# Kernel tuning notes

Measured on AMD Instinct MI355X. Metric: run time of the kernel, lower is better.

## Reference

```python
import jax, jax.numpy as jnp
import numpy as np

ATT_SCALE = 1.0  # att_scale_factor


def setup_inputs() -> dict:
    key = jax.random.key(0)
    k1, k2, k3, k4, k5 = jax.random.split(key, 5)
    B, P, IMG_D, SEQ_D, H = 64, 576, 1024, 1024, 512
    seq_features = jax.random.normal(k1, (B, SEQ_D), dtype=jnp.float32)
    img_features = jax.random.normal(k2, (B, P, IMG_D), dtype=jnp.float32)
    # torch nn.Linear weights: [out_features, in_features], scaled to typical init magnitude
    W_seq = jax.random.normal(k3, (H, SEQ_D), dtype=jnp.float32) * (1.0 / np.sqrt(SEQ_D))
    W_img = jax.random.normal(k4, (H, IMG_D), dtype=jnp.float32) * (1.0 / np.sqrt(IMG_D))
    W_w = jax.random.normal(k5, (1, H), dtype=jnp.float32) * (1.0 / np.sqrt(H))
    return {"seq_features": seq_features, "img_features": img_features,
            "W_seq": W_seq, "W_img": W_img, "W_w": W_w}


def reference(seq_features, img_features, W_seq, W_img, W_w):
    # tanh(SeqTrans(seq)) broadcast over patch dim (avoids explicit .repeat)
    seq_h = jnp.tanh(jnp.einsum('bd,hd->bh', seq_features, W_seq))          # [B, H]
    img_h = jnp.tanh(jnp.einsum('bpd,hd->bph', img_features, W_img))        # [B, P, H]
    attend = seq_h[:, None, :] * img_h                                       # [B, P, H]
    # Dropout is Identity (att_dropout=None)
    scores = ATT_SCALE * jnp.einsum('bph,oh->bpo', attend, W_w)              # [B, P, 1]
    alpha = jax.nn.softmax(scores, axis=1)                                   # softmax over patches
    # weighted sum over patches; alpha broadcasts over channel dim (no .repeat needed)
    attended_img = jnp.sum(img_features * alpha, axis=1)                     # [B, IMG_D]
    return attended_img
```

## Files before the change

kernel.cpp:

```cpp
#include <hip/hip_runtime.h>
#include <hip/hip_bf16.h>

#define BB 64
#define PP 576
#define DD 1024
#define HH 512

typedef __attribute__((ext_vector_type(4))) float f32x4;
typedef __attribute__((ext_vector_type(8))) short bf16x8;

__device__ __forceinline__ unsigned short f2bf(float f) {
    union { float f; unsigned u; } v; v.f = f;
    unsigned r = v.u + 0x7FFF + ((v.u >> 16) & 1);
    return (unsigned short)(r >> 16);
}

__device__ __forceinline__ float fast_tanh(float x) {
    float e = __expf(2.f * x);
    return 1.f - 2.f / (e + 1.f);
}

__device__ __forceinline__ void gload16(const void* g, void* l) {
    __builtin_amdgcn_global_load_lds((const __attribute__((address_space(1))) unsigned int*)g,
                                     (__attribute__((address_space(3))) unsigned int*)l,
                                     16, 0, 0);
}

__global__ __launch_bounds__(256) void k_convert(const float* __restrict__ w,
                                                 unsigned short* __restrict__ o) {
    int i = (blockIdx.x * 256 + threadIdx.x) * 4;
    f32x4 v = *(const f32x4*)(w + i);
    ushort4 r;
    r.x = f2bf(v.x); r.y = f2bf(v.y); r.z = f2bf(v.z); r.w = f2bf(v.w);
    *(ushort4*)(o + i) = r;
}

__global__ __launch_bounds__(128) void k_seq(const float* __restrict__ seq,
                                             const float* __restrict__ W_seq,
                                             const float* __restrict__ W_w,
                                             float* __restrict__ g) {
    int b = blockIdx.x;
    int h = blockIdx.y * 128 + threadIdx.x;
    __shared__ float s_seq[DD];
    #pragma unroll
    for (int i = 0; i < 8; i++) s_seq[threadIdx.x + i * 128] = seq[b * DD + threadIdx.x + i * 128];
    __syncthreads();
    const float* wr = W_seq + (size_t)h * DD;
    float acc = 0.f;
    #pragma unroll 4
    for (int d = 0; d < DD; d += 4) {
        f32x4 w4 = *(const f32x4*)(wr + d);
        acc += w4.x * s_seq[d] + w4.y * s_seq[d + 1] + w4.z * s_seq[d + 2] + w4.w * s_seq[d + 3];
    }
    g[b * HH + h] = fast_tanh(acc) * W_w[h];
}

__global__ __launch_bounds__(256) void k_scores(const float* __restrict__ img,
                                                const unsigned short* __restrict__ Wb,
                                                const float* __restrict__ g,
                                                float* __restrict__ sp) {
    int b = blockIdx.y;
    int rt = blockIdx.x % 9;
    int ch = blockIdx.x / 9;
    int p0 = rt * 64;
    int h0 = ch * 256;
    int tid = threadIdx.x;
    int w = tid >> 6, lane = tid & 63;

    __shared__ unsigned short As[2][64 * 64];
    __shared__ unsigned short Bs[2][256 * 64];

    float gr[4];
    #pragma unroll
    for (int n = 0; n < 4; ++n) gr[n] = g[b * HH + h0 + w * 64 + n * 16 + (lane & 15)];

    f32x4 acc[4][4];
    #pragma unroll
    for (int m = 0; m < 4; m++)
        #pragma unroll
        for (int n = 0; n < 4; n++) acc[m][n] = (f32x4)0.f;

    int ar = tid >> 2;
    int ac = (tid & 3) * 16;
    const float* asrc = img + ((size_t)(b * PP + p0 + ar)) * DD + ac;
    int cp = (tid & 3) * 2;
    int aw0 = ar * 64 + ((cp ^ (ar & 7)) * 8);
    int aw1 = ar * 64 + (((cp + 1) ^ (ar & 7)) * 8);

    int brow_l = lane >> 3;
    int bchunk = lane & 7;

    auto stageB = [&](int bi, int kr) {
        int k0 = kr * 64;
        #pragma unroll
        for (int i = 0; i < 8; ++i) {
            int hr = (w * 8 + i) * 8 + brow_l;
            const unsigned short* src = Wb + (size_t)(h0 + hr) * DD + k0 + ((bchunk ^ (hr & 7)) * 8);
            gload16(src, &Bs[bi][(w * 8 + i) * 512]);
        }
    };
    auto packA = [&](int bi, f32x4 v0, f32x4 v1, f32x4 v2, f32x4 v3) {
        bf16x8 pa, pb;
        pa[0] = (short)f2bf(v0.x); pa[1] = (short)f2bf(v0.y);
        pa[2] = (short)f2bf(v0.z); pa[3] = (short)f2bf(v0.w);
        pa[4] = (short)f2bf(v1.x); pa[5] = (short)f2bf(v1.y);
        pa[6] = (short)f2bf(v1.z); pa[7] = (short)f2bf(v1.w);
        pb[0] = (short)f2bf(v2.x); pb[1] = (short)f2bf(v2.y);
        pb[2] = (short)f2bf(v2.z); pb[3] = (short)f2bf(v2.w);
        pb[4] = (short)f2bf(v3.x); pb[5] = (short)f2bf(v3.y);
        pb[6] = (short)f2bf(v3.z); pb[7] = (short)f2bf(v3.w);
        *(bf16x8*)&As[bi][aw0] = pa;
        *(bf16x8*)&As[bi][aw1] = pb;
    };

    stageB(0, 0);
    {
        f32x4 v0 = *(const f32x4*)(asrc);
        f32x4 v1 = *(const f32x4*)(asrc + 4);
        f32x4 v2 = *(const f32x4*)(asrc + 8);
        f32x4 v3 = *(const f32x4*)(asrc + 12);
        packA(0, v0, v1, v2, v3);
    }
    __syncthreads();

    f32x4 va0, va1, va2, va3;
    for (int kr = 0; kr < 16; ++kr) {
        int cur = kr & 1, nxt = cur ^ 1;
        if (kr < 15) {
            stageB(nxt, kr + 1);
            int k0 = (kr + 1) * 64;
            va0 = *(const f32x4*)(asrc + k0);
            va1 = *(const f32x4*)(asrc + k0 + 4);
            va2 = *(const f32x4*)(asrc + k0 + 8);
            va3 = *(const f32x4*)(asrc + k0 + 12);
        }
        #pragma unroll
        for (int ks = 0; ks < 2; ++ks) {
            int cbase = ks * 4 + (lane >> 4);
            bf16x8 af[4], bfv[4];
            #pragma unroll
            for (int m = 0; m < 4; ++m) {
                int row = m * 16 + (lane & 15);
                af[m] = *(const bf16x8*)&As[cur][row * 64 + ((cbase ^ (row & 7)) * 8)];
            }
            #pragma unroll
            for (int n = 0; n < 4; ++n) {
                int hr = w * 64 + n * 16 + (lane & 15);
                bfv[n] = *(const bf16x8*)&Bs[cur][hr * 64 + ((cbase ^ (hr & 7)) * 8)];
            }
            #pragma unroll
            for (int m = 0; m < 4; ++m)
                #pragma unroll
                for (int n = 0; n < 4; ++n)
                    acc[m][n] = __builtin_amdgcn_mfma_f32_16x16x32_bf16(af[m], bfv[n], acc[m][n], 0, 0, 0);
        }
        if (kr < 15) packA(nxt, va0, va1, va2, va3);
        __syncthreads();
    }

    float part[4][4];
    #pragma unroll
    for (int m = 0; m < 4; m++)
        #pragma unroll
        for (int j = 0; j < 4; j++) part[m][j] = 0.f;
    #pragma unroll
    for (int m = 0; m < 4; ++m)
        #pragma unroll
        for (int n = 0; n < 4; ++n) {
            float gv = gr[n];
            f32x4 v = acc[m][n];
            #pragma unroll
            for (int j = 0; j < 4; ++j) part[m][j] += fast_tanh(v[j]) * gv;
        }
    #pragma unroll
    for (int mask = 1; mask < 16; mask <<= 1)
        #pragma unroll
        for (int m = 0; m < 4; ++m)
            #pragma unroll
            for (int j = 0; j < 4; ++j)
                part[m][j] += __shfl_xor(part[m][j], mask, 64);

    float* red = (float*)As;
    if ((lane & 15) == 0) {
        int hi = lane >> 4;
        #pragma unroll
        for (int m = 0; m < 4; ++m)
            #pragma unroll
            for (int j = 0; j < 4; ++j)
                red[w * 64 + m * 16 + hi * 4 + j] = part[m][j];
    }
    __syncthreads();
    if (tid < 64) {
        float s = red[tid] + red[64 + tid] + red[128 + tid] + red[192 + tid];
        sp[(size_t)ch * (BB * PP) + b * PP + p0 + tid] = s;
    }
}

__global__ __launch_bounds__(576) void k_softmax(const float* __restrict__ sp,
                                                 float* __restrict__ alpha) {
    int b = blockIdx.x;
    int t = threadIdx.x;
    __shared__ float red[9];
    float s = sp[b * PP + t] + sp[BB * PP + b * PP + t];
    float m = s;
    #pragma unroll
    for (int off = 32; off; off >>= 1) m = fmaxf(m, __shfl_xor(m, off, 64));
    int w = t >> 6;
    if ((t & 63) == 0) red[w] = m;
    __syncthreads();
    float gm = red[0];
    #pragma unroll
    for (int i = 1; i < 9; i++) gm = fmaxf(gm, red[i]);
    float e = __expf(s - gm);
    float sum = e;
    #pragma unroll
    for (int off = 32; off; off >>= 1) sum += __shfl_xor(sum, off, 64);
    __syncthreads();
    if ((t & 63) == 0) red[w] = sum;
    __syncthreads();
    float gsum = 0.f;
    #pragma unroll
    for (int i = 0; i < 9; i++) gsum += red[i];
    alpha[b * PP + t] = e / gsum;
}

__global__ __launch_bounds__(256) void k_attend(const float* __restrict__ img,
                                                const float* __restrict__ alpha,
                                                float* __restrict__ part) {
    int b = blockIdx.y;
    int pc = blockIdx.x;
    int t = threadIdx.x;
    __shared__ float al[64];
    if (t < 64) al[t] = alpha[b * PP + pc * 64 + t];
    __syncthreads();
    int d = t * 4;
    f32x4 acc = (f32x4)0.f;
    const float* base = img + ((size_t)b * PP + (size_t)pc * 64) * DD + d;
    #pragma unroll 4
    for (int i = 0; i < 64; i++) {
        f32x4 v = *(const f32x4*)(base + (size_t)i * DD);
        acc += al[i] * v;
    }
    float* o = part + ((size_t)pc * BB + b) * DD + d;
    *(f32x4*)o = acc;
}

__global__ __launch_bounds__(256) void k_reduce(const float* __restrict__ part,
                                                float* __restrict__ out) {
    int i = blockIdx.x * 256 + threadIdx.x;
    float s = 0.f;
    #pragma unroll
    for (int pc = 0; pc < 9; pc++) s += part[pc * (BB * DD) + i];
    out[i] = s;
}

extern "C" void kernel_launch(void* const* d_in, const int* in_sizes, int n_in,
                              void* d_out, int out_size, void* d_ws, size_t ws_size,
                              hipStream_t stream) {
    const float* seq   = (const float*)d_in[0];
    const float* img   = (const float*)d_in[1];
    const float* W_seq = (const float*)d_in[2];
    const float* W_img = (const float*)d_in[3];
    const float* W_w   = (const float*)d_in[4];
    float* out = (float*)d_out;

    char* ws = (char*)d_ws;
    unsigned short* Wb = (unsigned short*)ws;
    float* g      = (float*)(ws + 1048576);
    float* sp     = (float*)(ws + 1048576 + 131072);
    float* alpha  = (float*)(ws + 1048576 + 131072 + 294912);
    float* part   = (float*)(ws + 1048576 + 131072 + 294912 + 147456);

    k_convert<<<512, 256, 0, stream>>>(W_img, Wb);
    k_seq<<<dim3(BB, 4), 128, 0, stream>>>(seq, W_seq, W_w, g);
    k_scores<<<dim3(18, BB), 256, 0, stream>>>(img, Wb, g, sp);
    k_softmax<<<BB, 576, 0, stream>>>(sp, alpha);
    k_attend<<<dim3(9, BB), 256, 0, stream>>>(img, alpha, part);
    k_reduce<<<256, 256, 0, stream>>>(part, out);
}
```

Measured before the change: 152.3 us.

## Halve k_scores K-tile to 32 and hand-schedule loads with explicit waitcnt barriers

```diff
diff --git a/kernel.cpp b/kernel.cpp
--- a/kernel.cpp
+++ b/kernel.cpp
@@ -55,10 +55,10 @@
     g[b * HH + h] = fast_tanh(acc) * W_w[h];
 }
 
-__global__ __launch_bounds__(256) void k_scores(const float* __restrict__ img,
-                                                const unsigned short* __restrict__ Wb,
-                                                const float* __restrict__ g,
-                                                float* __restrict__ sp) {
+__global__ __launch_bounds__(256, 4) void k_scores(const float* __restrict__ img,
+                                                   const unsigned short* __restrict__ Wb,
+                                                   const float* __restrict__ g,
+                                                   float* __restrict__ sp) {
     int b = blockIdx.y;
     int rt = blockIdx.x % 9;
     int ch = blockIdx.x / 9;
@@ -67,8 +67,8 @@
     int tid = threadIdx.x;
     int w = tid >> 6, lane = tid & 63;
 
-    __shared__ unsigned short As[2][64 * 64];
-    __shared__ unsigned short Bs[2][256 * 64];
+    __shared__ unsigned short As[2][64 * 32];
+    __shared__ unsigned short Bs[2][256 * 32];
 
     float gr[4];
     #pragma unroll
@@ -80,82 +80,81 @@
         #pragma unroll
         for (int n = 0; n < 4; n++) acc[m][n] = (f32x4)0.f;
 
-    int ar = tid >> 2;
-    int ac = (tid & 3) * 16;
-    const float* asrc = img + ((size_t)(b * PP + p0 + ar)) * DD + ac;
-    int cp = (tid & 3) * 2;
-    int aw0 = ar * 64 + ((cp ^ (ar & 7)) * 8);
-    int aw1 = ar * 64 + (((cp + 1) ^ (ar & 7)) * 8);
-
-    int brow_l = lane >> 3;
-    int bchunk = lane & 7;
-
-    auto stageB = [&](int bi, int kr) {
-        int k0 = kr * 64;
-        #pragma unroll
-        for (int i = 0; i < 8; ++i) {
-            int hr = (w * 8 + i) * 8 + brow_l;
-            const unsigned short* src = Wb + (size_t)(h0 + hr) * DD + k0 + ((bchunk ^ (hr & 7)) * 8);
-            gload16(src, &Bs[bi][(w * 8 + i) * 512]);
-        }
-    };
-    auto packA = [&](int bi, f32x4 v0, f32x4 v1, f32x4 v2, f32x4 v3) {
-        bf16x8 pa, pb;
-        pa[0] = (short)f2bf(v0.x); pa[1] = (short)f2bf(v0.y);
-        pa[2] = (short)f2bf(v0.z); pa[3] = (short)f2bf(v0.w);
-        pa[4] = (short)f2bf(v1.x); pa[5] = (short)f2bf(v1.y);
-        pa[6] = (short)f2bf(v1.z); pa[7] = (short)f2bf(v1.w);
-        pb[0] = (short)f2bf(v2.x); pb[1] = (short)f2bf(v2.y);
-        pb[2] = (short)f2bf(v2.z); pb[3] = (short)f2bf(v2.w);
-        pb[4] = (short)f2bf(v3.x); pb[5] = (short)f2bf(v3.y);
-        pb[6] = (short)f2bf(v3.z); pb[7] = (short)f2bf(v3.w);
-        *(bf16x8*)&As[bi][aw0] = pa;
-        *(bf16x8*)&As[bi][aw1] = pb;
-    };
-
-    stageB(0, 0);
+    int arow = tid >> 2;
+    int acnk = tid & 3;
+    const float* asrc = img + ((size_t)(b * PP + p0 + arow)) * DD + acnk * 8;
+    int aw = arow * 32 + ((acnk ^ ((arow >> 1) & 3)) * 8);
+
+    int rl = lane >> 2;
+    int bswz = (lane & 3) ^ ((rl >> 1) & 3);
+    const unsigned short* bbase = Wb + (size_t)h0 * DD;
+
+    f32x4 u0, u1;
+
+    u0 = *(const f32x4*)(asrc);
+    u1 = *(const f32x4*)(asrc + 4);
+    __builtin_amdgcn_sched_barrier(0);
+    #pragma unroll
+    for (int i = 0; i < 4; ++i) {
+        int hr = w * 64 + i * 16 + rl;
+        gload16(bbase + (size_t)hr * DD + bswz * 8, &Bs[0][(w * 4 + i) * 512]);
+    }
+    asm volatile("s_waitcnt vmcnt(4)" ::: "memory");
     {
-        f32x4 v0 = *(const f32x4*)(asrc);
-        f32x4 v1 = *(const f32x4*)(asrc + 4);
-        f32x4 v2 = *(const f32x4*)(asrc + 8);
-        f32x4 v3 = *(const f32x4*)(asrc + 12);
-        packA(0, v0, v1, v2, v3);
-    }
-    __syncthreads();
-
-    f32x4 va0, va1, va2, va3;
-    for (int kr = 0; kr < 16; ++kr) {
+        bf16x8 p;
+        p[0] = (short)f2bf(u0.x); p[1] = (short)f2bf(u0.y);
+        p[2] = (short)f2bf(u0.z); p[3] = (short)f2bf(u0.w);
+        p[4] = (short)f2bf(u1.x); p[5] = (short)f2bf(u1.y);
+        p[6] = (short)f2bf(u1.z); p[7] = (short)f2bf(u1.w);
+        *(bf16x8*)&As[0][aw] = p;
+    }
+    asm volatile("s_waitcnt lgkmcnt(0)" ::: "memory");
+    __builtin_amdgcn_s_barrier();
+
+    int r15 = lane & 15;
+    int csw = (lane >> 4) ^ ((r15 >> 1) & 3);
+
+    for (int kr = 0; kr < 32; ++kr) {
         int cur = kr & 1, nxt = cur ^ 1;
-        if (kr < 15) {
-            stageB(nxt, kr + 1);
-            int k0 = (kr + 1) * 64;
-            va0 = *(const f32x4*)(asrc + k0);
-            va1 = *(const f32x4*)(asrc + k0 + 4);
-            va2 = *(const f32x4*)(asrc + k0 + 8);
-            va3 = *(const f32x4*)(asrc + k0 + 12);
-        }
-        #pragma unroll
-        for (int ks = 0; ks < 2; ++ks) {
-            int cbase = ks * 4 + (lane >> 4);
+        if (kr < 31) {
+            int k0 = (kr + 1) * 32;
+            u0 = *(const f32x4*)(asrc + k0);
+            u1 = *(const f32x4*)(asrc + k0 + 4);
+            __builtin_amdgcn_sched_barrier(0);
+            #pragma unroll
+            for (int i = 0; i < 4; ++i) {
+                int hr = w * 64 + i * 16 + rl;
+                gload16(bbase + (size_t)hr * DD + k0 + bswz * 8, &Bs[nxt][(w * 4 + i) * 512]);
+            }
+            asm volatile("s_waitcnt vmcnt(6)" ::: "memory");
+        } else {
+            asm volatile("s_waitcnt vmcnt(0)" ::: "memory");
+        }
+        {
             bf16x8 af[4], bfv[4];
             #pragma unroll
-            for (int m = 0; m < 4; ++m) {
-                int row = m * 16 + (lane & 15);
-                af[m] = *(const bf16x8*)&As[cur][row * 64 + ((cbase ^ (row & 7)) * 8)];
-            }
-            #pragma unroll
-            for (int n = 0; n < 4; ++n) {
-                int hr = w * 64 + n * 16 + (lane & 15);
-                bfv[n] = *(const bf16x8*)&Bs[cur][hr * 64 + ((cbase ^ (hr & 7)) * 8)];
-            }
+            for (int m = 0; m < 4; ++m)
+                af[m] = *(const bf16x8*)&As[cur][(m * 16 + r15) * 32 + csw * 8];
+            #pragma unroll
+            for (int n = 0; n < 4; ++n)
+                bfv[n] = *(const bf16x8*)&Bs[cur][(w * 64 + n * 16 + r15) * 32 + csw * 8];
             #pragma unroll
             for (int m = 0; m < 4; ++m)
                 #pragma unroll
                 for (int n = 0; n < 4; ++n)
                     acc[m][n] = __builtin_amdgcn_mfma_f32_16x16x32_bf16(af[m], bfv[n], acc[m][n], 0, 0, 0);
         }
-        if (kr < 15) packA(nxt, va0, va1, va2, va3);
-        __syncthreads();
+        if (kr < 31) {
+            asm volatile("s_waitcnt vmcnt(4)" ::: "memory");
+            bf16x8 p;
+            p[0] = (short)f2bf(u0.x); p[1] = (short)f2bf(u0.y);
+            p[2] = (short)f2bf(u0.z); p[3] = (short)f2bf(u0.w);
+            p[4] = (short)f2bf(u1.x); p[5] = (short)f2bf(u1.y);
+            p[6] = (short)f2bf(u1.z); p[7] = (short)f2bf(u1.w);
+            *(bf16x8*)&As[nxt][aw] = p;
+            asm volatile("s_waitcnt lgkmcnt(0)" ::: "memory");
+            __builtin_amdgcn_s_barrier();
+        }
     }
 
     float part[4][4];
@@ -180,7 +179,7 @@
             for (int j = 0; j < 4; ++j)
                 part[m][j] += __shfl_xor(part[m][j], mask, 64);
 
-    float* red = (float*)As;
+    float* red = (float*)&As[0][0];
     if ((lane & 15) == 0) {
         int hi = lane >> 4;
         #pragma unroll
```

After: 143.2 us. -6.0%, faster.
